# Kernel optimization log

Measured on AMD Instinct MI355X. Metric: run time of the kernel, lower is better.

The kernel has to match this reference:

```python
import jax, jax.numpy as jnp
import numpy as np

B, T = 1024, 64
DETER, STOCH, EMBED, ACT = 1024, 32, 1024, 32
HID = DETER  # hidden_size=None -> hid = deter_size
SCALE_LB = 0.1


def _init_linear(key, out_dim, in_dim):
    kw, kb = jax.random.split(key)
    bound = 1.0 / np.sqrt(in_dim)
    W = jax.random.uniform(kw, (out_dim, in_dim), jnp.float32, -bound, bound)
    b = jax.random.uniform(kb, (out_dim,), jnp.float32, -bound, bound)
    return W, b


def setup_inputs() -> dict:
    key = jax.random.key(0)
    ks = jax.random.split(key, 12)
    embeds = jax.random.normal(ks[0], (B, T, EMBED), jnp.float32)
    actions = jax.random.normal(ks[1], (B, T, ACT), jnp.float32)
    noise_prior = jax.random.normal(ks[2], (B, T, STOCH), jnp.float32)
    noise_post = jax.random.normal(ks[3], (B, T, STOCH), jnp.float32)
    deter0 = jnp.zeros((B, DETER), jnp.float32)
    stoch0 = jnp.zeros((B, STOCH), jnp.float32)
    # prior: action_state_projector
    asp_W, asp_b = _init_linear(ks[4], HID, STOCH + ACT)
    # prior: GRUCell (torch layout: 3*deter rows, gates r,z,n)
    gb = 1.0 / np.sqrt(DETER)
    k5a, k5b, k5c, k5d = jax.random.split(ks[5], 4)
    w_ih = jax.random.uniform(k5a, (3 * DETER, HID), jnp.float32, -gb, gb)
    w_hh = jax.random.uniform(k5b, (3 * DETER, DETER), jnp.float32, -gb, gb)
    b_ih = jax.random.uniform(k5c, (3 * DETER,), jnp.float32, -gb, gb)
    b_hh = jax.random.uniform(k5d, (3 * DETER,), jnp.float32, -gb, gb)
    # prior: rnn_to_prior_projector
    rp_W1, rp_b1 = _init_linear(ks[6], HID, DETER)
    rp_W2, rp_b2 = _init_linear(ks[7], 2 * STOCH, HID)
    # posterior mlp
    po_W1, po_b1 = _init_linear(ks[8], HID, DETER + EMBED)
    po_W2, po_b2 = _init_linear(ks[9], 2 * STOCH, HID)
    return dict(embeds=embeds, actions=actions, deter0=deter0, stoch0=stoch0,
                noise_prior=noise_prior, noise_post=noise_post,
                asp_W=asp_W, asp_b=asp_b, w_ih=w_ih, w_hh=w_hh, b_ih=b_ih, b_hh=b_hh,
                rp_W1=rp_W1, rp_b1=rp_b1, rp_W2=rp_W2, rp_b2=rp_b2,
                po_W1=po_W1, po_b1=po_b1, po_W2=po_W2, po_b2=po_b2)


def _observe(embeds, actions, deter0, stoch0, noise_prior, noise_post,
             asp_W, asp_b, w_ih, w_hh, b_ih, b_hh,
             rp_W1, rp_b1, rp_W2, rp_b2, po_W1, po_b1, po_W2, po_b2):
    def step(carry, xs):
        deter, stoch = carry
        a, e, n_pr, n_po = xs  # each (B, ...)
        # prior: action_state_projector
        h = jax.nn.elu(jnp.concatenate([stoch, a], axis=-1) @ asp_W.T + asp_b)
        # GRUCell (torch semantics)
        gi = h @ w_ih.T + b_ih          # (B, 3*DETER)
        gh = deter @ w_hh.T + b_hh      # (B, 3*DETER)
        i_r, i_z, i_n = jnp.split(gi, 3, axis=-1)
        h_r, h_z, h_n = jnp.split(gh, 3, axis=-1)
        r = jax.nn.sigmoid(i_r + h_r)
        z = jax.nn.sigmoid(i_z + h_z)
        n = jnp.tanh(i_n + r * h_n)
        deter = (1.0 - z) * n + z * deter
        # prior projector
        pr = jax.nn.elu(deter @ rp_W1.T + rp_b1) @ rp_W2.T + rp_b2
        p_mean, p_logstd = jnp.split(pr, 2, axis=-1)
        p_std = jax.nn.softplus(p_logstd) + SCALE_LB
        p_stoch = p_mean + n_pr * p_std
        # posterior
        po = jax.nn.elu(jnp.concatenate([deter, e], axis=-1) @ po_W1.T + po_b1) @ po_W2.T + po_b2
        q_mean, q_logstd = jnp.split(po, 2, axis=-1)
        q_std = jax.nn.softplus(q_logstd) + SCALE_LB
        q_stoch = q_mean + n_po * q_std
        return (deter, q_stoch), (q_mean, q_std, q_stoch, p_mean, p_std, p_stoch, deter)

    xs = (jnp.swapaxes(actions, 0, 1), jnp.swapaxes(embeds, 0, 1),
          jnp.swapaxes(noise_prior, 0, 1), jnp.swapaxes(noise_post, 0, 1))
    _, ys = jax.lax.scan(step, (deter0, stoch0), xs)
    # ys are time-major (T,B,...); return batch-major
    return tuple(jnp.swapaxes(y, 0, 1) for y in ys)


def reference(embeds, actions, deter0, stoch0, noise_prior, noise_post,
              asp_W, asp_b, w_ih, w_hh, b_ih, b_hh,
              rp_W1, rp_b1, rp_W2, rp_b2, po_W1, po_b1, po_W2, po_b2):
    # returns (post_mean, post_std, post_stoch, prior_mean, prior_std, prior_stoch, deter)
    return _observe(embeds, actions, deter0, stoch0, noise_prior, noise_post,
                    asp_W, asp_b, w_ih, w_hh, b_ih, b_hh,
                    rp_W1, rp_b1, rp_W2, rp_b2, po_W1, po_b1, po_W2, po_b2)
```

## Files before the change

kernel.cpp:

```cpp
#include <hip/hip_runtime.h>
#include <hip/hip_bf16.h>
#include <math.h>

typedef __bf16 bf16;
typedef bf16 bf16x8 __attribute__((ext_vector_type(8)));
typedef float f32x4 __attribute__((ext_vector_type(4)));

#define B_ 1024
#define T_ 64
#define D_ 1024
#define S_ 32
#define CH_ (B_*T_*S_)
#define DOFF_ ((size_t)6*CH_)

__device__ __forceinline__ float eluf(float x){ return x > 0.f ? x : expm1f(x); }
__device__ __forceinline__ float sigmoidf_(float x){ return 1.f/(1.f+expf(-x)); }
__device__ __forceinline__ float softplusf_(float x){
    return x > 0.f ? x + log1pf(expf(-x)) : log1pf(expf(x));
}

__device__ __forceinline__ void gload16(const bf16* g, bf16* l){
    __builtin_amdgcn_global_load_lds(
        (const __attribute__((address_space(1))) void*)(g),
        (__attribute__((address_space(3))) void*)(l), 16, 0, 0);
}

__global__ __launch_bounds__(256) void k_cvt(const float* __restrict__ src,
                                             bf16* __restrict__ dst, int n){
    int i = (blockIdx.x*256 + threadIdx.x)*4;
    if (i < n){
        float4 v = *reinterpret_cast<const float4*>(src + i);
        dst[i+0] = (bf16)v.x; dst[i+1] = (bf16)v.y;
        dst[i+2] = (bf16)v.z; dst[i+3] = (bf16)v.w;
    }
}

__global__ __launch_bounds__(256) void k_cvt_tr(const float* __restrict__ src,
                                                bf16* __restrict__ dst){
    int row = blockIdx.x;
    int b = row >> 6, t = row & 63;
    const float* s = src + (size_t)row*1024;
    bf16* d = dst + ((size_t)t*B_ + b)*1024;
    int i = threadIdx.x*4;
    float4 v = *reinterpret_cast<const float4*>(s + i);
    d[i+0] = (bf16)v.x; d[i+1] = (bf16)v.y;
    d[i+2] = (bf16)v.z; d[i+3] = (bf16)v.w;
}

__global__ __launch_bounds__(256) void k_h0(const float* __restrict__ stoch0,
                                            const float* __restrict__ actions,
                                            const float* __restrict__ aspW,
                                            const float* __restrict__ aspb,
                                            bf16* __restrict__ h_buf){
    int m = blockIdx.x;
    __shared__ float av[64];
    int tid = threadIdx.x;
    if (tid < 32)      av[tid] = stoch0[m*S_ + tid];
    else if (tid < 64) av[tid] = actions[(size_t)m*T_*S_ + (tid-32)];
    __syncthreads();
    for (int c = 0; c < 4; c++){
        int n = c*256 + tid;
        float s = aspb[n];
        const float* wr = aspW + n*64;
        #pragma unroll 8
        for (int k = 0; k < 64; k++) s += av[k]*wr[k];
        h_buf[(size_t)m*D_ + n] = (bf16)eluf(s);
    }
}

__global__ __launch_bounds__(256) void k_pre(const bf16* __restrict__ embf,
                                             const bf16* __restrict__ poW1,
                                             bf16* __restrict__ part){
    int m0 = blockIdx.x * 64;
    int tid = threadIdx.x;
    int w = tid >> 6, l = tid & 63;
    int lr = l & 15, ko = l >> 4;
    __shared__ bf16 Bl[2][16*64*8];
    int arow = m0 + w*16 + lr;
    const bf16* Ab = embf + (size_t)arow*1024 + ko*8;
    for (int sub = 0; sub < 4; sub++){
        int c0 = sub*256;
        const bf16* sp[4];
        #pragma unroll
        for (int p = 0; p < 4; p++){
            int s = p*256 + tid;
            int f = s >> 6, sl = s & 63;
            int col = c0 + f*16 + (sl & 15);
            sp[p] = poW1 + (size_t)col*2048 + 1024 + (sl >> 4)*8;
        }
        #pragma unroll
        for (int p = 0; p < 4; p++) gload16(sp[p], &Bl[0][(p*256 + tid)*8]);
        bf16x8 a = *(const bf16x8*)(Ab);
        __syncthreads();
        f32x4 acc[16] = {};
        for (int kt = 0; kt < 32; ++kt){
            int cur = kt & 1;
            if (kt < 31){
                int k1 = (kt+1)*32;
                #pragma unroll
                for (int p = 0; p < 4; p++)
                    gload16(sp[p] + k1, &Bl[cur ^ 1][(p*256 + tid)*8]);
            }
            bf16x8 an = a;
            if (kt < 31) an = *(const bf16x8*)(Ab + (kt+1)*32);
            const bf16* Br = &Bl[cur][0];
            #pragma unroll
            for (int f = 0; f < 16; f++){
                bf16x8 b = *(const bf16x8*)(&Br[((f*64) + l)*8]);
                acc[f] = __builtin_amdgcn_mfma_f32_16x16x32_bf16(a, b, acc[f], 0,0,0);
            }
            __syncthreads();
            a = an;
        }
        bf16* outT = &Bl[0][0];
        #pragma unroll
        for (int f = 0; f < 16; f++){
            int col = f*16 + lr;
            #pragma unroll
            for (int r = 0; r < 4; r++)
                outT[(w*16 + ko*4 + r)*256 + col] = (bf16)acc[f][r];
        }
        __syncthreads();
        {
            int colb = (tid & 31)*8;
            int rbase = tid >> 5;
            #pragma unroll
            for (int j = 0; j < 8; j++){
                int row = rbase + j*8;
                *(uint4*)&part[(size_t)(m0 + row)*1024 + c0 + colb] =
                    *(const uint4*)&outT[row*256 + colb];
            }
        }
        __syncthreads();
    }
}

__global__ __launch_bounds__(256) void k_gru(
        const bf16* __restrict__ h_buf, const bf16* __restrict__ dprev_b,
        const bf16* __restrict__ wih,   const bf16* __restrict__ whh,
        const float* __restrict__ bih,  const float* __restrict__ bhh,
        const float* __restrict__ dprev_f,
        float* __restrict__ dout_t, float* __restrict__ dcur_f,
        bf16* __restrict__ dcur_b,  bf16* __restrict__ dall_t){
    int bid = blockIdx.x;
    int n = bid & 31, mb = bid >> 5;
    int j0 = n*32, m0 = mb*64;
    int tid = threadIdx.x;
    int w = tid >> 6, l = tid & 63;
    int lr = l & 15, ko = l >> 4;
    __shared__ bf16 Bl[2][12*64*8];
    const bf16* sp[3];
    #pragma unroll
    for (int p = 0; p < 3; p++){
        int s = p*256 + tid;
        int f = s >> 6, sl = s & 63;
        int g = f >> 1, cfl = f & 1;
        int col = j0 + cfl*16 + (sl & 15);
        const bf16* base = (g < 3) ? wih : whh;
        int gg = (g < 3) ? g : g - 3;
        sp[p] = base + (size_t)(gg*1024 + col)*1024 + (sl >> 4)*8;
    }
    int arow = m0 + w*16 + lr;
    const bf16* hA = h_buf   + (size_t)arow*1024 + ko*8;
    const bf16* dA = dprev_b + (size_t)arow*1024 + ko*8;
    #pragma unroll
    for (int p = 0; p < 3; p++) gload16(sp[p], &Bl[0][(p*256 + tid)*8]);
    bf16x8 aH = *(const bf16x8*)(hA);
    bf16x8 aD = *(const bf16x8*)(dA);
    __syncthreads();
    f32x4 acc[6][2] = {};
    for (int kt = 0; kt < 32; ++kt){
        int cur = kt & 1;
        if (kt < 31){
            int k1 = (kt+1)*32;
            #pragma unroll
            for (int p = 0; p < 3; p++)
                gload16(sp[p] + k1, &Bl[cur ^ 1][(p*256 + tid)*8]);
        }
        bf16x8 aHn = aH, aDn = aD;
        if (kt < 31){
            aHn = *(const bf16x8*)(hA + (kt+1)*32);
            aDn = *(const bf16x8*)(dA + (kt+1)*32);
        }
        const bf16* Br = &Bl[cur][0];
        #pragma unroll
        for (int g = 0; g < 6; g++){
            #pragma unroll
            for (int cfl = 0; cfl < 2; cfl++){
                bf16x8 b = *(const bf16x8*)(&Br[((g*2 + cfl)*64 + l)*8]);
                acc[g][cfl] = __builtin_amdgcn_mfma_f32_16x16x32_bf16(
                    g < 3 ? aH : aD, b, acc[g][cfl], 0,0,0);
            }
        }
        __syncthreads();
        aH = aHn; aD = aDn;
    }
    #pragma unroll
    for (int cfl = 0; cfl < 2; cfl++){
        int j = j0 + cfl*16 + lr;
        float bir = bih[j],      bhr = bhh[j];
        float biz = bih[1024+j], bhz = bhh[1024+j];
        float bin = bih[2048+j], bhn = bhh[2048+j];
        #pragma unroll
        for (int r = 0; r < 4; r++){
            int m = m0 + w*16 + ko*4 + r;
            float ir  = acc[0][cfl][r] + bir;
            float iz  = acc[1][cfl][r] + biz;
            float in_ = acc[2][cfl][r] + bin;
            float hr  = acc[3][cfl][r] + bhr;
            float hz  = acc[4][cfl][r] + bhz;
            float hn  = acc[5][cfl][r] + bhn;
            float rg = sigmoidf_(ir + hr);
            float zg = sigmoidf_(iz + hz);
            float ng = tanhf(in_ + rg*hn);
            float dp = dprev_f[(size_t)m*D_ + j];
            float dn = (1.f - zg)*ng + zg*dp;
            dout_t[(size_t)m*(T_*D_) + j] = dn;
            dcur_f[(size_t)m*D_ + j] = dn;
            bf16 dnb = (bf16)dn;
            dcur_b[(size_t)m*D_ + j] = dnb;
            dall_t[(size_t)m*D_ + j] = dnb;
        }
    }
}

__global__ __launch_bounds__(256) void k_po1(
        const bf16* __restrict__ dcur_b,
        const bf16* __restrict__ poW1, const float* __restrict__ pob1,
        const bf16* __restrict__ partial, int t,
        bf16* __restrict__ po1h){
    int bid = blockIdx.x;
    int nn = bid & 31, mb = bid >> 5;
    int c0 = nn*32, m0 = mb*64;
    int tid = threadIdx.x;
    int w = tid >> 6, l = tid & 63;
    int lr = l & 15, ko = l >> 4;
    __shared__ bf16 Bl[2][4*64*8];
    const bf16* sp;
    {   int f = tid >> 6, sl = tid & 63;
        int ksub = f >> 1, cfl = f & 1;
        int col = c0 + cfl*16 + (sl & 15);
        sp = poW1 + (size_t)col*2048 + ksub*32 + (sl >> 4)*8;
    }
    int arow = m0 + w*16 + lr;
    const bf16* A = dcur_b + (size_t)arow*1024 + ko*8;
    gload16(sp, &Bl[0][tid*8]);
    bf16x8 a0 = *(const bf16x8*)(A);
    bf16x8 a1 = *(const bf16x8*)(A + 32);
    __syncthreads();
    f32x4 acc[2] = {};
    for (int kt = 0; kt < 16; ++kt){
        int cur = kt & 1;
        if (kt < 15) gload16(sp + (kt+1)*64, &Bl[cur ^ 1][tid*8]);
        bf16x8 a0n = a0, a1n = a1;
        if (kt < 15){
            a0n = *(const bf16x8*)(A + (kt+1)*64);
            a1n = *(const bf16x8*)(A + (kt+1)*64 + 32);
        }
        const bf16* Br = &Bl[cur][0];
        #pragma unroll
        for (int ksub = 0; ksub < 2; ksub++){
            #pragma unroll
            for (int cfl = 0; cfl < 2; cfl++){
                bf16x8 b = *(const bf16x8*)(&Br[((ksub*2 + cfl)*64 + l)*8]);
                acc[cfl] = __builtin_amdgcn_mfma_f32_16x16x32_bf16(
                    ksub ? a1 : a0, b, acc[cfl], 0,0,0);
            }
        }
        __syncthreads();
        a0 = a0n; a1 = a1n;
    }
    #pragma unroll
    for (int cfl = 0; cfl < 2; cfl++){
        int col = c0 + cfl*16 + lr;
        float bb = pob1[col];
        #pragma unroll
        for (int r = 0; r < 4; r++){
            int row = m0 + w*16 + ko*4 + r;
            float v = acc[cfl][r] + bb + (float)partial[((size_t)t*B_ + row)*1024 + col];
            po1h[(size_t)row*1024 + col] = (bf16)eluf(v);
        }
    }
}

__global__ __launch_bounds__(256) void k_po_out(
        const bf16* __restrict__ po1h,
        const bf16* __restrict__ poW2, const float* __restrict__ pob2,
        const float* __restrict__ noise_po, const float* __restrict__ actions,
        const bf16* __restrict__ aspW, const float* __restrict__ aspb,
        float* __restrict__ out, int t, bf16* __restrict__ h_next){
    int m0 = blockIdx.x * 16;
    int tid = threadIdx.x;
    int w = tid >> 6, l = tid & 63;
    int lr = l & 15, ko = l >> 4;
    __shared__ float ps[4][16][68];
    __shared__ bf16 smA[16][88];
    int ks = w * 256;
    f32x4 acc[4] = {};
    const bf16* apo = po1h + (size_t)(m0 + lr)*1024 + ks + ko*8;
    #pragma unroll
    for (int kk = 0; kk < 8; kk++){
        int k = kk*32;
        bf16x8 a2 = *(const bf16x8*)(apo + k);
        #pragma unroll
        for (int cf = 0; cf < 4; cf++){
            bf16x8 b2 = *(const bf16x8*)(poW2 + (size_t)(cf*16+lr)*1024 + ks + k + ko*8);
            acc[cf] = __builtin_amdgcn_mfma_f32_16x16x32_bf16(a2, b2, acc[cf], 0,0,0);
        }
    }
    #pragma unroll
    for (int cf = 0; cf < 4; cf++){
        int col = cf*16 + lr;
        #pragma unroll
        for (int r = 0; r < 4; r++) ps[w][ko*4+r][col] = acc[cf][r];
    }
    __syncthreads();
    for (int it = 0; it < 2; it++){
        int idx2 = tid + it*256;
        int s = idx2 & 31, mm = idx2 >> 5;
        int mg = m0 + mm;
        float qm  = ps[0][mm][s]    + ps[1][mm][s]    + ps[2][mm][s]    + ps[3][mm][s]    + pob2[s];
        float qls = ps[0][mm][32+s] + ps[1][mm][32+s] + ps[2][mm][32+s] + ps[3][mm][32+s] + pob2[32+s];
        float qstd = softplusf_(qls) + 0.1f;
        size_t no = (size_t)mg*(T_*S_) + (size_t)t*S_ + s;
        float qst = qm + noise_po[no]*qstd;
        out[0*(size_t)CH_ + no] = qm;
        out[1*(size_t)CH_ + no] = qstd;
        out[2*(size_t)CH_ + no] = qst;
        smA[mm][s] = (bf16)qst;
        if (t + 1 < T_)
            smA[mm][32+s] = (bf16)actions[(size_t)mg*(T_*S_) + (size_t)(t+1)*S_ + s];
    }
    __syncthreads();
    if (t + 1 < T_){
        #pragma unroll 4
        for (int c2 = 0; c2 < 16; c2++){
            int nb = w*256 + c2*16;
            f32x4 a2v = {0.f, 0.f, 0.f, 0.f};
            #pragma unroll
            for (int kk = 0; kk < 2; kk++){
                bf16x8 a = *(const bf16x8*)(&smA[lr][kk*32 + ko*8]);
                bf16x8 b = *(const bf16x8*)(aspW + (size_t)(nb+lr)*64 + kk*32 + ko*8);
                a2v = __builtin_amdgcn_mfma_f32_16x16x32_bf16(a, b, a2v, 0,0,0);
            }
            int n2 = nb + lr;
            float bb = aspb[n2];
            #pragma unroll
            for (int r = 0; r < 4; r++)
                h_next[(size_t)(m0 + ko*4 + r)*1024 + n2] = (bf16)eluf(a2v[r] + bb);
        }
    }
}

__global__ __launch_bounds__(256) void k_prior(
        const bf16* __restrict__ dallP, const bf16* __restrict__ dall0,
        const bf16* __restrict__ rpW1, const float* __restrict__ rpb1,
        const bf16* __restrict__ rpW2, const float* __restrict__ rpb2,
        const float* __restrict__ noise_pr,
        float* __restrict__ out){
    int bid = blockIdx.x;
    int sl = bid >> 4;
    int b0 = (bid & 15)*64;
    int t  = (sl == 63) ? 0 : sl + 1;
    const bf16* Abase = (sl == 63) ? dall0 : dallP + (size_t)sl*1048576;
    int tid = threadIdx.x;
    int w = tid >> 6, l = tid & 63;
    int lr = l & 15, ko = l >> 4;
    __shared__ bf16 Bl[2][8192];
    __shared__ bf16 rp1s[64][264];
    const bf16* Ar = Abase + (size_t)(b0 + w*16 + lr)*1024 + ko*8;
    f32x4 acc2[4] = {};
    const bf16* sp[4];
    {
        #pragma unroll
        for (int p = 0; p < 4; p++){
            int s = p*256 + tid;
            int f = s >> 6, sl2 = s & 63;
            int col = f*16 + (sl2 & 15);
            sp[p] = rpW1 + (size_t)col*1024 + (sl2 >> 4)*8;
        }
    }
    #pragma unroll
    for (int p = 0; p < 4; p++) gload16(sp[p], &Bl[0][(p*256 + tid)*8]);
    __syncthreads();
    for (int sub = 0; sub < 4; sub++){
        int c0 = sub*256;
        f32x4 acc[16] = {};
        bf16x8 a = *(const bf16x8*)(Ar);
        for (int kt = 0; kt < 32; ++kt){
            int cur = kt & 1;
            if (kt < 31){
                int k1 = (kt+1)*32;
                #pragma unroll
                for (int p = 0; p < 4; p++)
                    gload16(sp[p] + k1, &Bl[cur ^ 1][(p*256 + tid)*8]);
            }
            bf16x8 an = a;
            if (kt < 31) an = *(const bf16x8*)(Ar + (kt+1)*32);
            const bf16* Br = &Bl[cur][0];
            #pragma unroll
            for (int f = 0; f < 16; f++){
                bf16x8 b = *(const bf16x8*)(&Br[((f*64) + l)*8]);
                acc[f] = __builtin_amdgcn_mfma_f32_16x16x32_bf16(a, b, acc[f], 0,0,0);
            }
            __syncthreads();
            a = an;
        }
        if (sub < 3){
            int c1 = c0 + 256;
            #pragma unroll
            for (int p = 0; p < 4; p++){
                int s = p*256 + tid;
                int f = s >> 6, sl2 = s & 63;
                int col = c1 + f*16 + (sl2 & 15);
                sp[p] = rpW1 + (size_t)col*1024 + (sl2 >> 4)*8;
                gload16(sp[p], &Bl[0][(p*256 + tid)*8]);
            }
        }
        #pragma unroll
        for (int f = 0; f < 16; f++){
            int col = f*16 + lr;
            float bb = rpb1[c0 + col];
            #pragma unroll
            for (int r = 0; r < 4; r++)
                rp1s[w*16 + ko*4 + r][col] = (bf16)eluf(acc[f][r] + bb);
        }
        __syncthreads();
        #pragma unroll
        for (int kk = 0; kk < 8; kk++){
            int k = kk*32;
            bf16x8 a2 = *(const bf16x8*)(&rp1s[w*16 + lr][k + ko*8]);
            #pragma unroll
            for (int cf = 0; cf < 4; cf++){
                bf16x8 b2 = *(const bf16x8*)(rpW2 + (size_t)(cf*16+lr)*1024 + c0 + k + ko*8);
                acc2[cf] = __builtin_amdgcn_mfma_f32_16x16x32_bf16(a2, b2, acc2[cf], 0,0,0);
            }
        }
        __syncthreads();
    }
    #pragma unroll
    for (int cf = 0; cf < 2; cf++){
        int s = cf*16 + lr;
        float b1 = rpb2[s], b2 = rpb2[32+s];
        #pragma unroll
        for (int r = 0; r < 4; r++){
            int row = w*16 + ko*4 + r;
            float pm  = acc2[cf][r]   + b1;
            float pls = acc2[cf+2][r] + b2;
            float pstd = softplusf_(pls) + 0.1f;
            size_t no = (size_t)(b0 + row)*2048 + (size_t)t*32 + s;
            float pst = pm + noise_pr[no]*pstd;
            out[3*(size_t)CH_ + no] = pm;
            out[4*(size_t)CH_ + no] = pstd;
            out[5*(size_t)CH_ + no] = pst;
        }
    }
}

extern "C" void kernel_launch(void* const* d_in, const int* in_sizes, int n_in,
                              void* d_out, int out_size, void* d_ws, size_t ws_size,
                              hipStream_t stream) {
    const float* embeds   = (const float*)d_in[0];
    const float* actions  = (const float*)d_in[1];
    const float* deter0   = (const float*)d_in[2];
    const float* stoch0   = (const float*)d_in[3];
    const float* noise_pr = (const float*)d_in[4];
    const float* noise_po = (const float*)d_in[5];
    const float* asp_W    = (const float*)d_in[6];
    const float* asp_b    = (const float*)d_in[7];
    const float* w_ih     = (const float*)d_in[8];
    const float* w_hh     = (const float*)d_in[9];
    const float* b_ih     = (const float*)d_in[10];
    const float* b_hh     = (const float*)d_in[11];
    const float* rp_W1    = (const float*)d_in[12];
    const float* rp_b1    = (const float*)d_in[13];
    const float* rp_W2    = (const float*)d_in[14];
    const float* rp_b2    = (const float*)d_in[15];
    const float* po_W1    = (const float*)d_in[16];
    const float* po_b1    = (const float*)d_in[17];
    const float* po_W2    = (const float*)d_in[18];
    const float* po_b2    = (const float*)d_in[19];
    float* out = (float*)d_out;

    char* ws = (char*)d_ws;
    const size_t MB = 1024*1024;
    bf16*  h_buf   = (bf16*)(ws + 0*MB);
    bf16*  dbuf0   = (bf16*)(ws + 2*MB);
    bf16*  dbuf1   = (bf16*)(ws + 4*MB);
    bf16*  po1h    = (bf16*)(ws + 6*MB);
    float* dF0     = (float*)(ws + 10*MB);
    float* dF1     = (float*)(ws + 14*MB);
    bf16*  w_ih_b  = (bf16*)(ws + 18*MB);
    bf16*  w_hh_b  = (bf16*)(ws + 24*MB);
    bf16*  rpW1_b  = (bf16*)(ws + 30*MB);
    bf16*  poW1_b  = (bf16*)(ws + 32*MB);
    bf16*  rpW2_b  = (bf16*)(ws + 36*MB);
    bf16*  poW2_b  = (bf16*)(ws + 36*MB + 256*1024);
    bf16*  aspW_b  = (bf16*)(ws + 36*MB + 512*1024);
    bf16*  dall0   = (bf16*)(ws + 38*MB);
    bf16*  partial = (bf16*)(ws + 40*MB);
    bf16*  embf    = (bf16*)(out + DOFF_);
    bf16*  dbuf[2] = {dbuf0, dbuf1};
    float* dFb[2]  = {dF0, dF1};

    auto cvt = [&](const float* s, bf16* d, int n){
        k_cvt<<<(n/4 + 255)/256, 256, 0, stream>>>(s, d, n);
    };
    cvt(w_ih,  w_ih_b, 3072*1024);
    cvt(w_hh,  w_hh_b, 3072*1024);
    cvt(rp_W1, rpW1_b, 1024*1024);
    cvt(po_W1, poW1_b, 1024*2048);
    cvt(rp_W2, rpW2_b, 64*1024);
    cvt(po_W2, poW2_b, 64*1024);
    cvt(asp_W, aspW_b, 1024*64);
    cvt(deter0, dbuf0, 1024*1024);
    k_h0<<<1024, 256, 0, stream>>>(stoch0, actions, asp_W, asp_b, h_buf);
    k_cvt_tr<<<B_*T_, 256, 0, stream>>>(embeds, embf);
    k_pre<<<1024, 256, 0, stream>>>(embf, poW1_b, partial);

    for (int t = 0; t < T_; t++){
        const float* dprev_f = (t == 0) ? deter0 : dFb[t & 1];
        bf16* dall_t = (t == 0) ? dall0 : partial + (size_t)(t-1)*1048576;
        k_gru<<<512, 256, 0, stream>>>(h_buf, dbuf[t & 1], w_ih_b, w_hh_b,
                                       b_ih, b_hh, dprev_f,
                                       out + DOFF_ + (size_t)t*D_,
                                       dFb[(t+1) & 1], dbuf[(t+1) & 1], dall_t);
        k_po1<<<512, 256, 0, stream>>>(dbuf[(t+1) & 1], poW1_b, po_b1,
                                       partial, t, po1h);
        k_po_out<<<64, 256, 0, stream>>>(po1h, poW2_b, po_b2, noise_po, actions,
                                         aspW_b, asp_b, out, t, h_buf);
    }
    k_prior<<<1024, 256, 0, stream>>>(partial, dall0, rpW1_b, rp_b1,
                                      rpW2_b, rp_b2, noise_pr, out);
}
```

Baseline: 5.879 ms.

## Fuse per-timestep kernels into one persistent kernel with grid barriers

Replaces the three kernels launched per timestep (GRU, posterior hidden layer, posterior output and next input projection) with a single persistent kernel of 512 blocks that loops over time. Stages are separated by an atomic-counter grid barrier in workspace memory, reset with a memset before launch. This removes the launch gaps between the many small dependent kernels. It relies on all 512 blocks being co-resident and adds spin-wait barrier latency.

```diff
diff --git a/kernel.cpp b/kernel.cpp
--- a/kernel.cpp
+++ b/kernel.cpp
@@ -12,6 +12,7 @@
 #define S_ 32
 #define CH_ (B_*T_*S_)
 #define DOFF_ ((size_t)6*CH_)
+#define NBLK_ 512u
 
 __device__ __forceinline__ float eluf(float x){ return x > 0.f ? x : expm1f(x); }
 __device__ __forceinline__ float sigmoidf_(float x){ return 1.f/(1.f+expf(-x)); }
@@ -23,6 +24,18 @@
     __builtin_amdgcn_global_load_lds(
         (const __attribute__((address_space(1))) void*)(g),
         (__attribute__((address_space(3))) void*)(l), 16, 0, 0);
+}
+
+__device__ __forceinline__ void gridbar(unsigned* __restrict__ bar, int id){
+    __syncthreads();
+    if (threadIdx.x == 0){
+        unsigned* c = bar + (id << 4);
+        __hip_atomic_fetch_add(c, 1u, __ATOMIC_RELEASE, __HIP_MEMORY_SCOPE_AGENT);
+        while (__hip_atomic_load(c, __ATOMIC_RELAXED, __HIP_MEMORY_SCOPE_AGENT) < NBLK_)
+            __builtin_amdgcn_s_sleep(1);
+        __builtin_amdgcn_fence(__ATOMIC_ACQUIRE, "agent");
+    }
+    __syncthreads();
 }
 
 __global__ __launch_bounds__(256) void k_cvt(const float* __restrict__ src,
@@ -135,220 +148,238 @@
     }
 }
 
-__global__ __launch_bounds__(256) void k_gru(
-        const bf16* __restrict__ h_buf, const bf16* __restrict__ dprev_b,
-        const bf16* __restrict__ wih,   const bf16* __restrict__ whh,
-        const float* __restrict__ bih,  const float* __restrict__ bhh,
-        const float* __restrict__ dprev_f,
-        float* __restrict__ dout_t, float* __restrict__ dcur_f,
-        bf16* __restrict__ dcur_b,  bf16* __restrict__ dall_t){
+struct SArgs {
+    bf16* __restrict__ h_buf;
+    bf16* __restrict__ dbuf0;
+    bf16* __restrict__ dbuf1;
+    const bf16* __restrict__ wih;
+    const bf16* __restrict__ whh;
+    const float* __restrict__ bih;
+    const float* __restrict__ bhh;
+    const float* __restrict__ deter0;
+    float* __restrict__ dF0;
+    float* __restrict__ dF1;
+    float* __restrict__ out;
+    const bf16* __restrict__ poW1;
+    const float* __restrict__ pob1;
+    bf16* __restrict__ partial;
+    bf16* __restrict__ po1h;
+    const bf16* __restrict__ poW2;
+    const float* __restrict__ pob2;
+    const float* __restrict__ noise_po;
+    const float* __restrict__ actions;
+    const bf16* __restrict__ aspW;
+    const float* __restrict__ aspb;
+    bf16* __restrict__ dall0;
+    unsigned* __restrict__ bar;
+};
+
+__global__ __launch_bounds__(256, 2) void k_steps(SArgs a){
+    __shared__ __align__(16) char smem[24576];
     int bid = blockIdx.x;
-    int n = bid & 31, mb = bid >> 5;
-    int j0 = n*32, m0 = mb*64;
     int tid = threadIdx.x;
     int w = tid >> 6, l = tid & 63;
     int lr = l & 15, ko = l >> 4;
-    __shared__ bf16 Bl[2][12*64*8];
-    const bf16* sp[3];
+
+    int n = bid & 31, mb = bid >> 5;
+    int j0 = n*32, m0g = mb*64;
+    const bf16* spg[3];
     #pragma unroll
     for (int p = 0; p < 3; p++){
         int s = p*256 + tid;
         int f = s >> 6, sl = s & 63;
         int g = f >> 1, cfl = f & 1;
         int col = j0 + cfl*16 + (sl & 15);
-        const bf16* base = (g < 3) ? wih : whh;
+        const bf16* base = (g < 3) ? a.wih : a.whh;
         int gg = (g < 3) ? g : g - 3;
-        sp[p] = base + (size_t)(gg*1024 + col)*1024 + (sl >> 4)*8;
-    }
-    int arow = m0 + w*16 + lr;
-    const bf16* hA = h_buf   + (size_t)arow*1024 + ko*8;
-    const bf16* dA = dprev_b + (size_t)arow*1024 + ko*8;
-    #pragma unroll
-    for (int p = 0; p < 3; p++) gload16(sp[p], &Bl[0][(p*256 + tid)*8]);
-    bf16x8 aH = *(const bf16x8*)(hA);
-    bf16x8 aD = *(const bf16x8*)(dA);
-    __syncthreads();
-    f32x4 acc[6][2] = {};
-    for (int kt = 0; kt < 32; ++kt){
-        int cur = kt & 1;
-        if (kt < 31){
-            int k1 = (kt+1)*32;
-            #pragma unroll
-            for (int p = 0; p < 3; p++)
-                gload16(sp[p] + k1, &Bl[cur ^ 1][(p*256 + tid)*8]);
-        }
-        bf16x8 aHn = aH, aDn = aD;
-        if (kt < 31){
-            aHn = *(const bf16x8*)(hA + (kt+1)*32);
-            aDn = *(const bf16x8*)(dA + (kt+1)*32);
-        }
-        const bf16* Br = &Bl[cur][0];
-        #pragma unroll
-        for (int g = 0; g < 6; g++){
-            #pragma unroll
-            for (int cfl = 0; cfl < 2; cfl++){
-                bf16x8 b = *(const bf16x8*)(&Br[((g*2 + cfl)*64 + l)*8]);
-                acc[g][cfl] = __builtin_amdgcn_mfma_f32_16x16x32_bf16(
-                    g < 3 ? aH : aD, b, acc[g][cfl], 0,0,0);
-            }
-        }
-        __syncthreads();
-        aH = aHn; aD = aDn;
-    }
-    #pragma unroll
-    for (int cfl = 0; cfl < 2; cfl++){
-        int j = j0 + cfl*16 + lr;
-        float bir = bih[j],      bhr = bhh[j];
-        float biz = bih[1024+j], bhz = bhh[1024+j];
-        float bin = bih[2048+j], bhn = bhh[2048+j];
-        #pragma unroll
-        for (int r = 0; r < 4; r++){
-            int m = m0 + w*16 + ko*4 + r;
-            float ir  = acc[0][cfl][r] + bir;
-            float iz  = acc[1][cfl][r] + biz;
-            float in_ = acc[2][cfl][r] + bin;
-            float hr  = acc[3][cfl][r] + bhr;
-            float hz  = acc[4][cfl][r] + bhz;
-            float hn  = acc[5][cfl][r] + bhn;
-            float rg = sigmoidf_(ir + hr);
-            float zg = sigmoidf_(iz + hz);
-            float ng = tanhf(in_ + rg*hn);
-            float dp = dprev_f[(size_t)m*D_ + j];
-            float dn = (1.f - zg)*ng + zg*dp;
-            dout_t[(size_t)m*(T_*D_) + j] = dn;
-            dcur_f[(size_t)m*D_ + j] = dn;
-            bf16 dnb = (bf16)dn;
-            dcur_b[(size_t)m*D_ + j] = dnb;
-            dall_t[(size_t)m*D_ + j] = dnb;
-        }
-    }
-}
-
-__global__ __launch_bounds__(256) void k_po1(
-        const bf16* __restrict__ dcur_b,
-        const bf16* __restrict__ poW1, const float* __restrict__ pob1,
-        const bf16* __restrict__ partial, int t,
-        bf16* __restrict__ po1h){
-    int bid = blockIdx.x;
-    int nn = bid & 31, mb = bid >> 5;
-    int c0 = nn*32, m0 = mb*64;
-    int tid = threadIdx.x;
-    int w = tid >> 6, l = tid & 63;
-    int lr = l & 15, ko = l >> 4;
-    __shared__ bf16 Bl[2][4*64*8];
-    const bf16* sp;
+        spg[p] = base + (size_t)(gg*1024 + col)*1024 + (sl >> 4)*8;
+    }
+    int arow = m0g + w*16 + lr;
+    const bf16* hA = a.h_buf + (size_t)arow*1024 + ko*8;
+    const bf16* spp;
     {   int f = tid >> 6, sl = tid & 63;
         int ksub = f >> 1, cfl = f & 1;
-        int col = c0 + cfl*16 + (sl & 15);
-        sp = poW1 + (size_t)col*2048 + ksub*32 + (sl >> 4)*8;
-    }
-    int arow = m0 + w*16 + lr;
-    const bf16* A = dcur_b + (size_t)arow*1024 + ko*8;
-    gload16(sp, &Bl[0][tid*8]);
-    bf16x8 a0 = *(const bf16x8*)(A);
-    bf16x8 a1 = *(const bf16x8*)(A + 32);
-    __syncthreads();
-    f32x4 acc[2] = {};
-    for (int kt = 0; kt < 16; ++kt){
-        int cur = kt & 1;
-        if (kt < 15) gload16(sp + (kt+1)*64, &Bl[cur ^ 1][tid*8]);
-        bf16x8 a0n = a0, a1n = a1;
-        if (kt < 15){
-            a0n = *(const bf16x8*)(A + (kt+1)*64);
-            a1n = *(const bf16x8*)(A + (kt+1)*64 + 32);
-        }
-        const bf16* Br = &Bl[cur][0];
-        #pragma unroll
-        for (int ksub = 0; ksub < 2; ksub++){
+        int col = j0 + cfl*16 + (sl & 15);
+        spp = a.poW1 + (size_t)col*2048 + ksub*32 + (sl >> 4)*8;
+    }
+
+    int sync_id = 0;
+    for (int t = 0; t < T_; t++){
+        {
+            const float* dprev_f = (t == 0) ? a.deter0 : ((t & 1) ? a.dF1 : a.dF0);
+            float* dcur_f = (((t+1) & 1)) ? a.dF1 : a.dF0;
+            const bf16* dprev_bp = (t & 1) ? a.dbuf1 : a.dbuf0;
+            bf16* dcur_bp = (((t+1) & 1)) ? a.dbuf1 : a.dbuf0;
+            float* dout_t = a.out + DOFF_ + (size_t)t*D_;
+            bf16* dall_t = (t == 0) ? a.dall0 : a.partial + (size_t)(t-1)*1048576;
+            bf16 (*Bl)[6144] = (bf16(*)[6144])smem;
+            const bf16* dA = dprev_bp + (size_t)arow*1024 + ko*8;
+            #pragma unroll
+            for (int p = 0; p < 3; p++) gload16(spg[p], &Bl[0][(p*256 + tid)*8]);
+            bf16x8 aH = *(const bf16x8*)(hA);
+            bf16x8 aD = *(const bf16x8*)(dA);
+            __syncthreads();
+            f32x4 acc[6][2] = {};
+            for (int kt = 0; kt < 32; ++kt){
+                int cur = kt & 1;
+                if (kt < 31){
+                    int k1 = (kt+1)*32;
+                    #pragma unroll
+                    for (int p = 0; p < 3; p++)
+                        gload16(spg[p] + k1, &Bl[cur ^ 1][(p*256 + tid)*8]);
+                }
+                bf16x8 aHn = aH, aDn = aD;
+                if (kt < 31){
+                    aHn = *(const bf16x8*)(hA + (kt+1)*32);
+                    aDn = *(const bf16x8*)(dA + (kt+1)*32);
+                }
+                const bf16* Br = &Bl[cur][0];
+                #pragma unroll
+                for (int g = 0; g < 6; g++){
+                    #pragma unroll
+                    for (int cfl = 0; cfl < 2; cfl++){
+                        bf16x8 b = *(const bf16x8*)(&Br[((g*2 + cfl)*64 + l)*8]);
+                        acc[g][cfl] = __builtin_amdgcn_mfma_f32_16x16x32_bf16(
+                            g < 3 ? aH : aD, b, acc[g][cfl], 0,0,0);
+                    }
+                }
+                __syncthreads();
+                aH = aHn; aD = aDn;
+            }
             #pragma unroll
             for (int cfl = 0; cfl < 2; cfl++){
-                bf16x8 b = *(const bf16x8*)(&Br[((ksub*2 + cfl)*64 + l)*8]);
-                acc[cfl] = __builtin_amdgcn_mfma_f32_16x16x32_bf16(
-                    ksub ? a1 : a0, b, acc[cfl], 0,0,0);
-            }
-        }
-        __syncthreads();
-        a0 = a0n; a1 = a1n;
-    }
-    #pragma unroll
-    for (int cfl = 0; cfl < 2; cfl++){
-        int col = c0 + cfl*16 + lr;
-        float bb = pob1[col];
-        #pragma unroll
-        for (int r = 0; r < 4; r++){
-            int row = m0 + w*16 + ko*4 + r;
-            float v = acc[cfl][r] + bb + (float)partial[((size_t)t*B_ + row)*1024 + col];
-            po1h[(size_t)row*1024 + col] = (bf16)eluf(v);
-        }
-    }
-}
-
-__global__ __launch_bounds__(256) void k_po_out(
-        const bf16* __restrict__ po1h,
-        const bf16* __restrict__ poW2, const float* __restrict__ pob2,
-        const float* __restrict__ noise_po, const float* __restrict__ actions,
-        const bf16* __restrict__ aspW, const float* __restrict__ aspb,
-        float* __restrict__ out, int t, bf16* __restrict__ h_next){
-    int m0 = blockIdx.x * 16;
-    int tid = threadIdx.x;
-    int w = tid >> 6, l = tid & 63;
-    int lr = l & 15, ko = l >> 4;
-    __shared__ float ps[4][16][68];
-    __shared__ bf16 smA[16][88];
-    int ks = w * 256;
-    f32x4 acc[4] = {};
-    const bf16* apo = po1h + (size_t)(m0 + lr)*1024 + ks + ko*8;
-    #pragma unroll
-    for (int kk = 0; kk < 8; kk++){
-        int k = kk*32;
-        bf16x8 a2 = *(const bf16x8*)(apo + k);
-        #pragma unroll
-        for (int cf = 0; cf < 4; cf++){
-            bf16x8 b2 = *(const bf16x8*)(poW2 + (size_t)(cf*16+lr)*1024 + ks + k + ko*8);
-            acc[cf] = __builtin_amdgcn_mfma_f32_16x16x32_bf16(a2, b2, acc[cf], 0,0,0);
-        }
-    }
-    #pragma unroll
-    for (int cf = 0; cf < 4; cf++){
-        int col = cf*16 + lr;
-        #pragma unroll
-        for (int r = 0; r < 4; r++) ps[w][ko*4+r][col] = acc[cf][r];
-    }
-    __syncthreads();
-    for (int it = 0; it < 2; it++){
-        int idx2 = tid + it*256;
-        int s = idx2 & 31, mm = idx2 >> 5;
-        int mg = m0 + mm;
-        float qm  = ps[0][mm][s]    + ps[1][mm][s]    + ps[2][mm][s]    + ps[3][mm][s]    + pob2[s];
-        float qls = ps[0][mm][32+s] + ps[1][mm][32+s] + ps[2][mm][32+s] + ps[3][mm][32+s] + pob2[32+s];
-        float qstd = softplusf_(qls) + 0.1f;
-        size_t no = (size_t)mg*(T_*S_) + (size_t)t*S_ + s;
-        float qst = qm + noise_po[no]*qstd;
-        out[0*(size_t)CH_ + no] = qm;
-        out[1*(size_t)CH_ + no] = qstd;
-        out[2*(size_t)CH_ + no] = qst;
-        smA[mm][s] = (bf16)qst;
-        if (t + 1 < T_)
-            smA[mm][32+s] = (bf16)actions[(size_t)mg*(T_*S_) + (size_t)(t+1)*S_ + s];
-    }
-    __syncthreads();
-    if (t + 1 < T_){
-        #pragma unroll 4
-        for (int c2 = 0; c2 < 16; c2++){
-            int nb = w*256 + c2*16;
-            f32x4 a2v = {0.f, 0.f, 0.f, 0.f};
-            #pragma unroll
-            for (int kk = 0; kk < 2; kk++){
-                bf16x8 a = *(const bf16x8*)(&smA[lr][kk*32 + ko*8]);
-                bf16x8 b = *(const bf16x8*)(aspW + (size_t)(nb+lr)*64 + kk*32 + ko*8);
-                a2v = __builtin_amdgcn_mfma_f32_16x16x32_bf16(a, b, a2v, 0,0,0);
-            }
-            int n2 = nb + lr;
-            float bb = aspb[n2];
-            #pragma unroll
-            for (int r = 0; r < 4; r++)
-                h_next[(size_t)(m0 + ko*4 + r)*1024 + n2] = (bf16)eluf(a2v[r] + bb);
-        }
+                int j = j0 + cfl*16 + lr;
+                float bir = a.bih[j],      bhr = a.bhh[j];
+                float biz = a.bih[1024+j], bhz = a.bhh[1024+j];
+                float bin = a.bih[2048+j], bhn = a.bhh[2048+j];
+                #pragma unroll
+                for (int r = 0; r < 4; r++){
+                    int m = m0g + w*16 + ko*4 + r;
+                    float ir  = acc[0][cfl][r] + bir;
+                    float iz  = acc[1][cfl][r] + biz;
+                    float in_ = acc[2][cfl][r] + bin;
+                    float hr  = acc[3][cfl][r] + bhr;
+                    float hz  = acc[4][cfl][r] + bhz;
+                    float hn  = acc[5][cfl][r] + bhn;
+                    float rg = sigmoidf_(ir + hr);
+                    float zg = sigmoidf_(iz + hz);
+                    float ng = tanhf(in_ + rg*hn);
+                    float dp = dprev_f[(size_t)m*D_ + j];
+                    float dn = (1.f - zg)*ng + zg*dp;
+                    dout_t[(size_t)m*(T_*D_) + j] = dn;
+                    dcur_f[(size_t)m*D_ + j] = dn;
+                    bf16 dnb = (bf16)dn;
+                    dcur_bp[(size_t)m*D_ + j] = dnb;
+                    dall_t[(size_t)m*D_ + j] = dnb;
+                }
+            }
+        }
+        gridbar(a.bar, sync_id++);
+        {
+            const bf16* dcur_bp = (((t+1) & 1)) ? a.dbuf1 : a.dbuf0;
+            bf16 (*Bl)[2048] = (bf16(*)[2048])smem;
+            const bf16* A = dcur_bp + (size_t)arow*1024 + ko*8;
+            gload16(spp, &Bl[0][tid*8]);
+            bf16x8 a0 = *(const bf16x8*)(A);
+            bf16x8 a1 = *(const bf16x8*)(A + 32);
+            __syncthreads();
+            f32x4 acc[2] = {};
+            for (int kt = 0; kt < 16; ++kt){
+                int cur = kt & 1;
+                if (kt < 15) gload16(spp + (kt+1)*64, &Bl[cur ^ 1][tid*8]);
+                bf16x8 a0n = a0, a1n = a1;
+                if (kt < 15){
+                    a0n = *(const bf16x8*)(A + (kt+1)*64);
+                    a1n = *(const bf16x8*)(A + (kt+1)*64 + 32);
+                }
+                const bf16* Br = &Bl[cur][0];
+                #pragma unroll
+                for (int ksub = 0; ksub < 2; ksub++){
+                    #pragma unroll
+                    for (int cfl = 0; cfl < 2; cfl++){
+                        bf16x8 b = *(const bf16x8*)(&Br[((ksub*2 + cfl)*64 + l)*8]);
+                        acc[cfl] = __builtin_amdgcn_mfma_f32_16x16x32_bf16(
+                            ksub ? a1 : a0, b, acc[cfl], 0,0,0);
+                    }
+                }
+                __syncthreads();
+                a0 = a0n; a1 = a1n;
+            }
+            #pragma unroll
+            for (int cfl = 0; cfl < 2; cfl++){
+                int col = j0 + cfl*16 + lr;
+                float bb = a.pob1[col];
+                #pragma unroll
+                for (int r = 0; r < 4; r++){
+                    int row = m0g + w*16 + ko*4 + r;
+                    float v = acc[cfl][r] + bb +
+                              (float)a.partial[((size_t)t*B_ + row)*1024 + col];
+                    a.po1h[(size_t)row*1024 + col] = (bf16)eluf(v);
+                }
+            }
+        }
+        gridbar(a.bar, sync_id++);
+        if (bid < 64){
+            int m0 = bid << 4;
+            float (*ps)[16][68] = (float(*)[16][68])smem;
+            bf16 (*smA)[88] = (bf16(*)[88])(smem + 17408);
+            int ks = w * 256;
+            f32x4 acc[4] = {};
+            const bf16* apo = a.po1h + (size_t)(m0 + lr)*1024 + ks + ko*8;
+            #pragma unroll
+            for (int kk = 0; kk < 8; kk++){
+                int k = kk*32;
+                bf16x8 a2 = *(const bf16x8*)(apo + k);
+                #pragma unroll
+                for (int cf = 0; cf < 4; cf++){
+                    bf16x8 b2 = *(const bf16x8*)(a.poW2 + (size_t)(cf*16+lr)*1024 + ks + k + ko*8);
+                    acc[cf] = __builtin_amdgcn_mfma_f32_16x16x32_bf16(a2, b2, acc[cf], 0,0,0);
+                }
+            }
+            #pragma unroll
+            for (int cf = 0; cf < 4; cf++){
+                int col = cf*16 + lr;
+                #pragma unroll
+                for (int r = 0; r < 4; r++) ps[w][ko*4+r][col] = acc[cf][r];
+            }
+            __syncthreads();
+            for (int it = 0; it < 2; it++){
+                int idx2 = tid + it*256;
+                int s = idx2 & 31, mm = idx2 >> 5;
+                int mg = m0 + mm;
+                float qm  = ps[0][mm][s]    + ps[1][mm][s]    + ps[2][mm][s]    + ps[3][mm][s]    + a.pob2[s];
+                float qls = ps[0][mm][32+s] + ps[1][mm][32+s] + ps[2][mm][32+s] + ps[3][mm][32+s] + a.pob2[32+s];
+                float qstd = softplusf_(qls) + 0.1f;
+                size_t no = (size_t)mg*(T_*S_) + (size_t)t*S_ + s;
+                float qst = qm + a.noise_po[no]*qstd;
+                a.out[0*(size_t)CH_ + no] = qm;
+                a.out[1*(size_t)CH_ + no] = qstd;
+                a.out[2*(size_t)CH_ + no] = qst;
+                smA[mm][s] = (bf16)qst;
+                if (t + 1 < T_)
+                    smA[mm][32+s] = (bf16)a.actions[(size_t)mg*(T_*S_) + (size_t)(t+1)*S_ + s];
+            }
+            __syncthreads();
+            if (t + 1 < T_){
+                #pragma unroll 4
+                for (int c2 = 0; c2 < 16; c2++){
+                    int nb = w*256 + c2*16;
+                    f32x4 a2v = {0.f, 0.f, 0.f, 0.f};
+                    #pragma unroll
+                    for (int kk = 0; kk < 2; kk++){
+                        bf16x8 av = *(const bf16x8*)(&smA[lr][kk*32 + ko*8]);
+                        bf16x8 bv = *(const bf16x8*)(a.aspW + (size_t)(nb+lr)*64 + kk*32 + ko*8);
+                        a2v = __builtin_amdgcn_mfma_f32_16x16x32_bf16(av, bv, a2v, 0,0,0);
+                    }
+                    int n2 = nb + lr;
+                    float bb = a.aspb[n2];
+                    #pragma unroll
+                    for (int r = 0; r < 4; r++)
+                        a.h_buf[(size_t)(m0 + ko*4 + r)*1024 + n2] = (bf16)eluf(a2v[r] + bb);
+                }
+            }
+        }
+        gridbar(a.bar, sync_id++);
     }
 }
 
@@ -497,11 +528,12 @@
     bf16*  rpW2_b  = (bf16*)(ws + 36*MB);
     bf16*  poW2_b  = (bf16*)(ws + 36*MB + 256*1024);
     bf16*  aspW_b  = (bf16*)(ws + 36*MB + 512*1024);
+    unsigned* bar  = (unsigned*)(ws + 37*MB);
     bf16*  dall0   = (bf16*)(ws + 38*MB);
     bf16*  partial = (bf16*)(ws + 40*MB);
     bf16*  embf    = (bf16*)(out + DOFF_);
-    bf16*  dbuf[2] = {dbuf0, dbuf1};
-    float* dFb[2]  = {dF0, dF1};
+
+    hipMemsetAsync(bar, 0, 192*64, stream);
 
     auto cvt = [&](const float* s, bf16* d, int n){
         k_cvt<<<(n/4 + 255)/256, 256, 0, stream>>>(s, d, n);
@@ -518,18 +550,24 @@
     k_cvt_tr<<<B_*T_, 256, 0, stream>>>(embeds, embf);
     k_pre<<<1024, 256, 0, stream>>>(embf, poW1_b, partial);
 
-    for (int t = 0; t < T_; t++){
-        const float* dprev_f = (t == 0) ? deter0 : dFb[t & 1];
-        bf16* dall_t = (t == 0) ? dall0 : partial + (size_t)(t-1)*1048576;
-        k_gru<<<512, 256, 0, stream>>>(h_buf, dbuf[t & 1], w_ih_b, w_hh_b,
-                                       b_ih, b_hh, dprev_f,
-                                       out + DOFF_ + (size_t)t*D_,
-                                       dFb[(t+1) & 1], dbuf[(t+1) & 1], dall_t);
-        k_po1<<<512, 256, 0, stream>>>(dbuf[(t+1) & 1], poW1_b, po_b1,
-                                       partial, t, po1h);
-        k_po_out<<<64, 256, 0, stream>>>(po1h, poW2_b, po_b2, noise_po, actions,
-                                         aspW_b, asp_b, out, t, h_buf);
-    }
+    SArgs sa;
+    sa.h_buf = h_buf;  sa.dbuf0 = dbuf0;  sa.dbuf1 = dbuf1;
+    sa.wih = w_ih_b;   sa.whh = w_hh_b;
+    sa.bih = b_ih;     sa.bhh = b_hh;
+    sa.deter0 = deter0;
+    sa.dF0 = dF0;      sa.dF1 = dF1;
+    sa.out = out;
+    sa.poW1 = poW1_b;  sa.pob1 = po_b1;
+    sa.partial = partial;
+    sa.po1h = po1h;
+    sa.poW2 = poW2_b;  sa.pob2 = po_b2;
+    sa.noise_po = noise_po;
+    sa.actions = actions;
+    sa.aspW = aspW_b;  sa.aspb = asp_b;
+    sa.dall0 = dall0;
+    sa.bar = bar;
+    k_steps<<<512, 256, 0, stream>>>(sa);
+
     k_prior<<<1024, 256, 0, stream>>>(partial, dall0, rpW1_b, rp_b1,
                                       rpW2_b, rp_b2, noise_pr, out);
 }
```

New measurement: 14.66 ms. +149.3%, slower.
